# Optimization experiments

Hardware: AMD Instinct MI355X
Metric: run time of the kernel (lower is better)

The kernel has to match this reference:

```python
import jax, jax.numpy as jnp
import numpy as np

NB, M, FIN = 8, 32768, 32       # batch, mesh vertices, input features
RANK, FILT = 5, 32              # Chebyshev order, output filters
E = 262144                      # nnz of rescaled Laplacian (~8 per row)


def setup_inputs() -> dict:
    key = jax.random.key(0)
    ks = jax.random.split(key, 6)
    x = jax.random.normal(ks[0], (NB, M, FIN), dtype=jnp.float32)
    rows = jax.random.randint(ks[1], (E,), 0, M, dtype=jnp.int32)
    cols = jax.random.randint(ks[2], (E,), 0, M, dtype=jnp.int32)
    # rescaled-Laplacian values, roughly spectral-normalized
    vals = jax.random.normal(ks[3], (E,), dtype=jnp.float32) * np.float32(1.0 / np.sqrt(8.0))
    kernel = jax.random.normal(ks[4], (FIN * RANK, FILT), dtype=jnp.float32) * np.float32(0.05)
    bias = jnp.zeros((FILT,), dtype=jnp.float32)
    return {"x": x, "vals": vals, "kernel": kernel, "bias": bias, "rows": rows, "cols": cols}


def _spmm(rows, cols, vals, x0):
    # y[m, f, n] = sum_j L[m, j] * x0[j, f, n]   (COO SpMM via gather + segment_sum)
    g = vals[:, None, None] * x0[cols]           # [E, Fin, N]
    return jax.ops.segment_sum(g, rows, num_segments=x0.shape[0])


def reference(x, vals, kernel, bias, rows, cols):
    N, Mm, Fin = x.shape
    x0 = jnp.transpose(x, (1, 2, 0))             # [M, Fin, N]
    xs = [x0]
    x1 = x0
    if RANK > 1:
        x1 = _spmm(rows, cols, vals, x0)         # T_1 = L x
        xs.append(x1)
    for _ in range(2, RANK):                     # T_k = 2 L T_{k-1} - T_{k-2}
        x2 = 2.0 * _spmm(rows, cols, vals, x1) - x0
        xs.append(x2)
        x0, x1 = x1, x2
    xk = jnp.stack(xs, axis=0)                   # [K, M, Fin, N]
    xk = jnp.transpose(xk, (3, 1, 2, 0)).reshape(N * Mm, Fin * RANK)  # Fin-major, rank inner
    out = xk @ kernel + bias                     # [N*M, FILT]
    return out.reshape(N, Mm, FILT)
```

## Files before the change

### kernel.cpp

```cpp
#include <hip/hip_runtime.h>

#define M_VERT 32768
#define NBATCH 8
#define FIN 32
#define RANK 5
#define FILT 32
#define E_NNZ 262144
#define ROWLEN 256
#define EPAD (E_NNZ + 7 * M_VERT)

typedef short short8 __attribute__((ext_vector_type(8)));
typedef float f32x4 __attribute__((ext_vector_type(4)));

__device__ __forceinline__ float bfl(unsigned int u) {
    unsigned int x = u << 16; return __builtin_bit_cast(float, x);
}
__device__ __forceinline__ float bfh(unsigned int u) {
    unsigned int x = u & 0xffff0000u; return __builtin_bit_cast(float, x);
}
__device__ __forceinline__ unsigned int f2bf(float f) {
    unsigned int x = __builtin_bit_cast(unsigned int, f);
    return (x + 0x7fffu + ((x >> 16) & 1u)) >> 16;
}
__device__ __forceinline__ unsigned int pk(float a, float b) {
    return f2bf(a) | (f2bf(b) << 16);
}


__global__ void hist_kernel(const int* __restrict__ rows, int* __restrict__ cnt) {
    int e = blockIdx.x * blockDim.x + threadIdx.x;
    if (e < E_NNZ) atomicAdd(&cnt[rows[e]], 1);
}

__global__ __launch_bounds__(1024) void scan_kernel(const int* __restrict__ cnt,
                                                    int* __restrict__ rp,
                                                    int* __restrict__ fill) {
    __shared__ int sums[1024];
    int t = threadIdx.x;
    int base = t * 32;
    int local[32];
    int s = 0;
#pragma unroll
    for (int i = 0; i < 32; ++i) {
        int c = (cnt[base + i] + 7) & ~7;
        local[i] = c; s += c;
    }
    sums[t] = s;
    __syncthreads();
    for (int off = 1; off < 1024; off <<= 1) {
        int add = (t >= off) ? sums[t - off] : 0;
        __syncthreads();
        sums[t] += add;
        __syncthreads();
    }
    int pre = (t == 0) ? 0 : sums[t - 1];
#pragma unroll
    for (int i = 0; i < 32; ++i) { rp[base + i] = pre; pre += local[i]; }
    if (t == 1023) rp[M_VERT] = pre;
#pragma unroll
    for (int i = 0; i < 32; ++i) fill[base + i] = 0;
}

__global__ void scatter_kernel(const int* __restrict__ rows, const int* __restrict__ cols,
                               const float* __restrict__ vals, const int* __restrict__ rp,
                               int* __restrict__ fill, int2* __restrict__ ev) {
    int e = blockIdx.x * blockDim.x + threadIdx.x;
    if (e < E_NNZ) {
        int r = rows[e];
        int pos = rp[r] + atomicAdd(&fill[r], 1);
        int2 p; p.x = cols[e]; p.y = __builtin_bit_cast(int, vals[e]);
        ev[pos] = p;
    }
}


__global__ void pack_kernel(const float* __restrict__ x, unsigned short* __restrict__ T0) {
    int tid = blockIdx.x * blockDim.x + threadIdx.x;
    int m = tid >> 5;
    int r = tid & 31;
    int n = r >> 2;
    int q = r & 3;
    const float* src = x + ((size_t)n * M_VERT + m) * FIN + q * 8;
    float4 v0 = *(const float4*)(src);
    float4 v1 = *(const float4*)(src + 4);
    uint4 u;
    u.x = pk(v0.x, v0.y); u.y = pk(v0.z, v0.w);
    u.z = pk(v1.x, v1.y); u.w = pk(v1.z, v1.w);
    *(uint4*)(T0 + (size_t)m * ROWLEN + n * FIN + q * 8) = u;
}


__global__ void packw_kernel(const float* __restrict__ W, unsigned short* __restrict__ Wb) {
    int idx = blockIdx.x * blockDim.x + threadIdx.x;
    if (idx >= 640) return;
    int lane = idx & 63;
    int kf = idx >> 6;
    int k = kf >> 1, ft = kf & 1;
    int f = ft * 16 + (lane & 15);
    int fin0 = (lane >> 4) * 8;
    unsigned short tmp[8];
#pragma unroll
    for (int j = 0; j < 8; ++j)
        tmp[j] = (unsigned short)f2bf(W[((fin0 + j) * RANK + k) * FILT + f]);
    uint4 u;
    u.x = (unsigned int)tmp[0] | ((unsigned int)tmp[1] << 16);
    u.y = (unsigned int)tmp[2] | ((unsigned int)tmp[3] << 16);
    u.z = (unsigned int)tmp[4] | ((unsigned int)tmp[5] << 16);
    u.w = (unsigned int)tmp[6] | ((unsigned int)tmp[7] << 16);
    *(uint4*)(Wb + (size_t)idx * 8) = u;
}


__global__ __launch_bounds__(256) void spmm_kernel(const int* __restrict__ rp,
                                                   const int2* __restrict__ ev,
                                                   const unsigned short* __restrict__ Tin,
                                                   const unsigned short* __restrict__ Tsub,
                                                   unsigned short* __restrict__ Tout, int cheb) {
    int w = threadIdx.x >> 6;
    int l = threadIdx.x & 63;
    int m = blockIdx.x * 4 + w;
    int col = l * 4;
    int s = __builtin_amdgcn_readfirstlane(rp[m]);
    int e = __builtin_amdgcn_readfirstlane(rp[m + 1]);
    float a0 = 0.f, a1 = 0.f, a2 = 0.f, a3 = 0.f;
    for (int j = s; j < e; j += 8) {
        int2 ed[8];
        uint2 t[8];
#pragma unroll
        for (int i = 0; i < 8; ++i) ed[i] = ev[j + i];
#pragma unroll
        for (int i = 0; i < 8; ++i)
            t[i] = *(const uint2*)(Tin + (size_t)ed[i].x * ROWLEN + col);
#pragma unroll
        for (int i = 0; i < 8; ++i) {
            float v = __builtin_bit_cast(float, ed[i].y);
            a0 += v * bfl(t[i].x); a1 += v * bfh(t[i].x);
            a2 += v * bfl(t[i].y); a3 += v * bfh(t[i].y);
        }
    }
    if (cheb) {
        uint2 o = *(const uint2*)(Tsub + (size_t)m * ROWLEN + col);
        a0 = 2.f * a0 - bfl(o.x); a1 = 2.f * a1 - bfh(o.x);
        a2 = 2.f * a2 - bfl(o.y); a3 = 2.f * a3 - bfh(o.y);
    }
    uint2 r;
    r.x = pk(a0, a1); r.y = pk(a2, a3);
    *(uint2*)(Tout + (size_t)m * ROWLEN + col) = r;
}


__global__ __launch_bounds__(256) void gemm_kernel(const unsigned short* __restrict__ T0,
                                                   const unsigned short* __restrict__ T1,
                                                   const unsigned short* __restrict__ T2,
                                                   const unsigned short* __restrict__ T3,
                                                   const unsigned short* __restrict__ T4,
                                                   const unsigned short* __restrict__ Wb,
                                                   const float* __restrict__ bias,
                                                   float* __restrict__ out) {
    int w = threadIdx.x >> 6;
    int l = threadIdx.x & 63;
    int n  = blockIdx.x & 7;
    int mb = blockIdx.x >> 3;
    int m0 = (mb * 4 + w) * 16;
    int lrow = l & 15;
    int quad = l >> 4;

    short8 bfrag[5][2];
#pragma unroll
    for (int kf = 0; kf < 10; ++kf)
        bfrag[kf >> 1][kf & 1] = *(const short8*)(Wb + ((size_t)kf * 64 + l) * 8);

    float b0 = bias[lrow];
    float b1 = bias[16 + lrow];

    const unsigned short* Ts[5] = {T0, T1, T2, T3, T4};
    size_t abase = (size_t)(m0 + lrow) * ROWLEN + quad * 8 + n * FIN;

    f32x4 c0 = {0.f, 0.f, 0.f, 0.f};
    f32x4 c1 = {0.f, 0.f, 0.f, 0.f};
#pragma unroll
    for (int k = 0; k < 5; ++k) {
        short8 a = *(const short8*)(Ts[k] + abase);
        c0 = __builtin_amdgcn_mfma_f32_16x16x32_bf16(a, bfrag[k][0], c0, 0, 0, 0);
        c1 = __builtin_amdgcn_mfma_f32_16x16x32_bf16(a, bfrag[k][1], c1, 0, 0, 0);
    }
    float* op = out + ((size_t)n * M_VERT + m0) * FILT;
#pragma unroll
    for (int r = 0; r < 4; ++r) {
        int orow = quad * 4 + r;
        op[(size_t)orow * FILT + lrow]      = c0[r] + b0;
        op[(size_t)orow * FILT + 16 + lrow] = c1[r] + b1;
    }
}


extern "C" void kernel_launch(void* const* d_in, const int* in_sizes, int n_in,
                              void* d_out, int out_size, void* d_ws, size_t ws_size,
                              hipStream_t stream) {
    const float* x    = (const float*)d_in[0];
    const float* vals = (const float*)d_in[1];
    const float* W    = (const float*)d_in[2];
    const float* bias = (const float*)d_in[3];
    const int*   rows = (const int*)d_in[4];
    const int*   cols = (const int*)d_in[5];
    float* out = (float*)d_out;

    const size_t TSZ = (size_t)M_VERT * ROWLEN;
    unsigned short* T0 = (unsigned short*)d_ws;
    unsigned short* T1 = T0 + TSZ;
    unsigned short* T2 = T1 + TSZ;
    unsigned short* T3 = T2 + TSZ;
    unsigned short* T4 = T3 + TSZ;
    int*  rp   = (int*)(T4 + TSZ);
    int*  fill = rp + (M_VERT + 2);
    int2* ev   = (int2*)(fill + M_VERT);
    unsigned short* Wb = (unsigned short*)(ev + EPAD);

    hipMemsetAsync(fill, 0, M_VERT * sizeof(int), stream);
    hipMemsetAsync(ev, 0, (size_t)EPAD * sizeof(int2), stream);
    hist_kernel<<<E_NNZ / 256, 256, 0, stream>>>(rows, fill);
    scan_kernel<<<1, 1024, 0, stream>>>(fill, rp, fill);
    scatter_kernel<<<E_NNZ / 256, 256, 0, stream>>>(rows, cols, vals, rp, fill, ev);
    packw_kernel<<<3, 256, 0, stream>>>(W, Wb);
    pack_kernel<<<M_VERT * 32 / 256, 256, 0, stream>>>(x, T0);

    spmm_kernel<<<M_VERT / 4, 256, 0, stream>>>(rp, ev, T0, T0, T1, 0);
    spmm_kernel<<<M_VERT / 4, 256, 0, stream>>>(rp, ev, T1, T0, T2, 1);
    spmm_kernel<<<M_VERT / 4, 256, 0, stream>>>(rp, ev, T2, T1, T3, 1);
    spmm_kernel<<<M_VERT / 4, 256, 0, stream>>>(rp, ev, T3, T2, T4, 1);

    gemm_kernel<<<(M_VERT / 64) * 8, 256, 0, stream>>>(T0, T1, T2, T3, T4, Wb, bias, out);
}
```

Measured before the change: 264.4 us.

## Switch Chebyshev intermediates to batch-major slices and per-batch SpMM gathers

```diff
diff --git a/kernel.cpp b/kernel.cpp
--- a/kernel.cpp
+++ b/kernel.cpp
@@ -6,8 +6,8 @@
 #define RANK 5
 #define FILT 32
 #define E_NNZ 262144
-#define ROWLEN 256
 #define EPAD (E_NNZ + 7 * M_VERT)
+#define SLICE ((size_t)M_VERT * FIN)
 
 typedef short short8 __attribute__((ext_vector_type(8)));
 typedef float f32x4 __attribute__((ext_vector_type(4)));
@@ -75,18 +75,14 @@
 
 
 __global__ void pack_kernel(const float* __restrict__ x, unsigned short* __restrict__ T0) {
-    int tid = blockIdx.x * blockDim.x + threadIdx.x;
-    int m = tid >> 5;
-    int r = tid & 31;
-    int n = r >> 2;
-    int q = r & 3;
-    const float* src = x + ((size_t)n * M_VERT + m) * FIN + q * 8;
+    size_t tid = (size_t)blockIdx.x * blockDim.x + threadIdx.x;
+    const float* src = x + tid * 8;
     float4 v0 = *(const float4*)(src);
     float4 v1 = *(const float4*)(src + 4);
     uint4 u;
     u.x = pk(v0.x, v0.y); u.y = pk(v0.z, v0.w);
     u.z = pk(v1.x, v1.y); u.w = pk(v1.z, v1.w);
-    *(uint4*)(T0 + (size_t)m * ROWLEN + n * FIN + q * 8) = u;
+    *(uint4*)(T0 + tid * 8) = u;
 }
 
 
@@ -111,56 +107,75 @@
 }
 
 
-__global__ __launch_bounds__(256) void spmm_kernel(const int* __restrict__ rp,
-                                                   const int2* __restrict__ ev,
-                                                   const unsigned short* __restrict__ Tin,
-                                                   const unsigned short* __restrict__ Tsub,
-                                                   unsigned short* __restrict__ Tout, int cheb) {
+__global__ __launch_bounds__(256) void spmmn_kernel(const int* __restrict__ rp,
+                                                    const int2* __restrict__ ev,
+                                                    const unsigned short* __restrict__ Tin,
+                                                    const unsigned short* __restrict__ Tsub,
+                                                    unsigned short* __restrict__ Tout, int cheb) {
+    int t = threadIdx.x;
+    int g = t >> 3;
+    int p = t & 7;
+    int n  = blockIdx.x >> 10;
+    int rb = blockIdx.x & 1023;
+    int m = rb * 32 + g;
+    const unsigned short* Tn = Tin + (size_t)n * SLICE;
+    int s = rp[m], e = rp[m + 1];
+    float a0 = 0.f, a1 = 0.f, a2 = 0.f, a3 = 0.f;
+    for (int j = s; j < e; j += 8) {
+        uint4 e0 = *(const uint4*)(ev + j);
+        uint4 e1 = *(const uint4*)(ev + j + 2);
+        uint4 e2 = *(const uint4*)(ev + j + 4);
+        uint4 e3 = *(const uint4*)(ev + j + 6);
+        uint2 t0 = *(const uint2*)(Tn + (size_t)e0.x * FIN + p * 4);
+        uint2 t1 = *(const uint2*)(Tn + (size_t)e0.z * FIN + p * 4);
+        uint2 t2 = *(const uint2*)(Tn + (size_t)e1.x * FIN + p * 4);
+        uint2 t3 = *(const uint2*)(Tn + (size_t)e1.z * FIN + p * 4);
+        uint2 t4 = *(const uint2*)(Tn + (size_t)e2.x * FIN + p * 4);
+        uint2 t5 = *(const uint2*)(Tn + (size_t)e2.z * FIN + p * 4);
+        uint2 t6 = *(const uint2*)(Tn + (size_t)e3.x * FIN + p * 4);
+        uint2 t7 = *(const uint2*)(Tn + (size_t)e3.z * FIN + p * 4);
+        float v;
+        v = __builtin_bit_cast(float, e0.y);
+        a0 += v * bfl(t0.x); a1 += v * bfh(t0.x); a2 += v * bfl(t0.y); a3 += v * bfh(t0.y);
+        v = __builtin_bit_cast(float, e0.w);
+        a0 += v * bfl(t1.x); a1 += v * bfh(t1.x); a2 += v * bfl(t1.y); a3 += v * bfh(t1.y);
+        v = __builtin_bit_cast(float, e1.y);
+        a0 += v * bfl(t2.x); a1 += v * bfh(t2.x); a2 += v * bfl(t2.y); a3 += v * bfh(t2.y);
+        v = __builtin_bit_cast(float, e1.w);
+        a0 += v * bfl(t3.x); a1 += v * bfh(t3.x); a2 += v * bfl(t3.y); a3 += v * bfh(t3.y);
+        v = __builtin_bit_cast(float, e2.y);
+        a0 += v * bfl(t4.x); a1 += v * bfh(t4.x); a2 += v * bfl(t4.y); a3 += v * bfh(t4.y);
+        v = __builtin_bit_cast(float, e2.w);
+        a0 += v * bfl(t5.x); a1 += v * bfh(t5.x); a2 += v * bfl(t5.y); a3 += v * bfh(t5.y);
+        v = __builtin_bit_cast(float, e3.y);
+        a0 += v * bfl(t6.x); a1 += v * bfh(t6.x); a2 += v * bfl(t6.y); a3 += v * bfh(t6.y);
+        v = __builtin_bit_cast(float, e3.w);
+        a0 += v * bfl(t7.x); a1 += v * bfh(t7.x); a2 += v * bfl(t7.y); a3 += v * bfh(t7.y);
+    }
+    size_t off = (size_t)n * SLICE + (size_t)m * FIN + p * 4;
+    if (cheb) {
+        uint2 o = *(const uint2*)(Tsub + off);
+        a0 = 2.f * a0 - bfl(o.x); a1 = 2.f * a1 - bfh(o.x);
+        a2 = 2.f * a2 - bfl(o.y); a3 = 2.f * a3 - bfh(o.y);
+    }
+    uint2 r;
+    r.x = pk(a0, a1); r.y = pk(a2, a3);
+    *(uint2*)(Tout + off) = r;
+}
+
+
+__global__ __launch_bounds__(256, 4) void gemm_kernel(const unsigned short* __restrict__ T0,
+                                                      const unsigned short* __restrict__ T1,
+                                                      const unsigned short* __restrict__ T2,
+                                                      const unsigned short* __restrict__ T3,
+                                                      const unsigned short* __restrict__ T4,
+                                                      const unsigned short* __restrict__ Wb,
+                                                      const float* __restrict__ bias,
+                                                      float* __restrict__ out) {
     int w = threadIdx.x >> 6;
     int l = threadIdx.x & 63;
-    int m = blockIdx.x * 4 + w;
-    int col = l * 4;
-    int s = __builtin_amdgcn_readfirstlane(rp[m]);
-    int e = __builtin_amdgcn_readfirstlane(rp[m + 1]);
-    float a0 = 0.f, a1 = 0.f, a2 = 0.f, a3 = 0.f;
-    for (int j = s; j < e; j += 8) {
-        int2 ed[8];
-        uint2 t[8];
-#pragma unroll
-        for (int i = 0; i < 8; ++i) ed[i] = ev[j + i];
-#pragma unroll
-        for (int i = 0; i < 8; ++i)
-            t[i] = *(const uint2*)(Tin + (size_t)ed[i].x * ROWLEN + col);
-#pragma unroll
-        for (int i = 0; i < 8; ++i) {
-            float v = __builtin_bit_cast(float, ed[i].y);
-            a0 += v * bfl(t[i].x); a1 += v * bfh(t[i].x);
-            a2 += v * bfl(t[i].y); a3 += v * bfh(t[i].y);
-        }
-    }
-    if (cheb) {
-        uint2 o = *(const uint2*)(Tsub + (size_t)m * ROWLEN + col);
-        a0 = 2.f * a0 - bfl(o.x); a1 = 2.f * a1 - bfh(o.x);
-        a2 = 2.f * a2 - bfl(o.y); a3 = 2.f * a3 - bfh(o.y);
-    }
-    uint2 r;
-    r.x = pk(a0, a1); r.y = pk(a2, a3);
-    *(uint2*)(Tout + (size_t)m * ROWLEN + col) = r;
-}
-
-
-__global__ __launch_bounds__(256) void gemm_kernel(const unsigned short* __restrict__ T0,
-                                                   const unsigned short* __restrict__ T1,
-                                                   const unsigned short* __restrict__ T2,
-                                                   const unsigned short* __restrict__ T3,
-                                                   const unsigned short* __restrict__ T4,
-                                                   const unsigned short* __restrict__ Wb,
-                                                   const float* __restrict__ bias,
-                                                   float* __restrict__ out) {
-    int w = threadIdx.x >> 6;
-    int l = threadIdx.x & 63;
-    int n  = blockIdx.x & 7;
-    int mb = blockIdx.x >> 3;
+    int g  = blockIdx.x & 1;
+    int mb = blockIdx.x >> 1;
     int m0 = (mb * 4 + w) * 16;
     int lrow = l & 15;
     int quad = l >> 4;
@@ -174,22 +189,39 @@
     float b1 = bias[16 + lrow];
 
     const unsigned short* Ts[5] = {T0, T1, T2, T3, T4};
-    size_t abase = (size_t)(m0 + lrow) * ROWLEN + quad * 8 + n * FIN;
-
-    f32x4 c0 = {0.f, 0.f, 0.f, 0.f};
-    f32x4 c1 = {0.f, 0.f, 0.f, 0.f};
+    size_t rowoff = (size_t)(m0 + lrow) * FIN + quad * 8;
+
+    f32x4 c0[4], c1[4];
+#pragma unroll
+    for (int nn = 0; nn < 4; ++nn) { c0[nn] = (f32x4){0.f,0.f,0.f,0.f}; c1[nn] = (f32x4){0.f,0.f,0.f,0.f}; }
+
 #pragma unroll
     for (int k = 0; k < 5; ++k) {
-        short8 a = *(const short8*)(Ts[k] + abase);
-        c0 = __builtin_amdgcn_mfma_f32_16x16x32_bf16(a, bfrag[k][0], c0, 0, 0, 0);
-        c1 = __builtin_amdgcn_mfma_f32_16x16x32_bf16(a, bfrag[k][1], c1, 0, 0, 0);
-    }
-    float* op = out + ((size_t)n * M_VERT + m0) * FILT;
-#pragma unroll
-    for (int r = 0; r < 4; ++r) {
-        int orow = quad * 4 + r;
-        op[(size_t)orow * FILT + lrow]      = c0[r] + b0;
-        op[(size_t)orow * FILT + 16 + lrow] = c1[r] + b1;
+        const unsigned short* p = Ts[k] + rowoff + (size_t)g * 4 * SLICE;
+        short8 a0 = *(const short8*)(p);
+        short8 a1 = *(const short8*)(p + SLICE);
+        short8 a2 = *(const short8*)(p + 2 * SLICE);
+        short8 a3 = *(const short8*)(p + 3 * SLICE);
+        c0[0] = __builtin_amdgcn_mfma_f32_16x16x32_bf16(a0, bfrag[k][0], c0[0], 0, 0, 0);
+        c1[0] = __builtin_amdgcn_mfma_f32_16x16x32_bf16(a0, bfrag[k][1], c1[0], 0, 0, 0);
+        c0[1] = __builtin_amdgcn_mfma_f32_16x16x32_bf16(a1, bfrag[k][0], c0[1], 0, 0, 0);
+        c1[1] = __builtin_amdgcn_mfma_f32_16x16x32_bf16(a1, bfrag[k][1], c1[1], 0, 0, 0);
+        c0[2] = __builtin_amdgcn_mfma_f32_16x16x32_bf16(a2, bfrag[k][0], c0[2], 0, 0, 0);
+        c1[2] = __builtin_amdgcn_mfma_f32_16x16x32_bf16(a2, bfrag[k][1], c1[2], 0, 0, 0);
+        c0[3] = __builtin_amdgcn_mfma_f32_16x16x32_bf16(a3, bfrag[k][0], c0[3], 0, 0, 0);
+        c1[3] = __builtin_amdgcn_mfma_f32_16x16x32_bf16(a3, bfrag[k][1], c1[3], 0, 0, 0);
+    }
+
+#pragma unroll
+    for (int nn = 0; nn < 4; ++nn) {
+        int n = g * 4 + nn;
+        float* op = out + ((size_t)n * M_VERT + m0) * FILT;
+#pragma unroll
+        for (int r = 0; r < 4; ++r) {
+            int orow = quad * 4 + r;
+            op[(size_t)orow * FILT + lrow]      = c0[nn][r] + b0;
+            op[(size_t)orow * FILT + 16 + lrow] = c1[nn][r] + b1;
+        }
     }
 }
 
@@ -205,7 +237,7 @@
     const int*   cols = (const int*)d_in[5];
     float* out = (float*)d_out;
 
-    const size_t TSZ = (size_t)M_VERT * ROWLEN;
+    const size_t TSZ = (size_t)NBATCH * SLICE;
     unsigned short* T0 = (unsigned short*)d_ws;
     unsigned short* T1 = T0 + TSZ;
     unsigned short* T2 = T1 + TSZ;
@@ -213,7 +245,7 @@
     unsigned short* T4 = T3 + TSZ;
     int*  rp   = (int*)(T4 + TSZ);
     int*  fill = rp + (M_VERT + 2);
-    int2* ev   = (int2*)(fill + M_VERT);
+    int2* ev   = (int2*)(((uintptr_t)(fill + M_VERT) + 15) & ~(uintptr_t)15);
     unsigned short* Wb = (unsigned short*)(ev + EPAD);
 
     hipMemsetAsync(fill, 0, M_VERT * sizeof(int), stream);
@@ -222,12 +254,12 @@
     scan_kernel<<<1, 1024, 0, stream>>>(fill, rp, fill);
     scatter_kernel<<<E_NNZ / 256, 256, 0, stream>>>(rows, cols, vals, rp, fill, ev);
     packw_kernel<<<3, 256, 0, stream>>>(W, Wb);
-    pack_kernel<<<M_VERT * 32 / 256, 256, 0, stream>>>(x, T0);
-
-    spmm_kernel<<<M_VERT / 4, 256, 0, stream>>>(rp, ev, T0, T0, T1, 0);
-    spmm_kernel<<<M_VERT / 4, 256, 0, stream>>>(rp, ev, T1, T0, T2, 1);
-    spmm_kernel<<<M_VERT / 4, 256, 0, stream>>>(rp, ev, T2, T1, T3, 1);
-    spmm_kernel<<<M_VERT / 4, 256, 0, stream>>>(rp, ev, T3, T2, T4, 1);
-
-    gemm_kernel<<<(M_VERT / 64) * 8, 256, 0, stream>>>(T0, T1, T2, T3, T4, Wb, bias, out);
-}
+    pack_kernel<<<(NBATCH * M_VERT * FIN / 8) / 256, 256, 0, stream>>>(x, T0);
+
+    spmmn_kernel<<<NBATCH * 1024, 256, 0, stream>>>(rp, ev, T0, T0, T1, 0);
+    spmmn_kernel<<<NBATCH * 1024, 256, 0, stream>>>(rp, ev, T1, T0, T2, 1);
+    spmmn_kernel<<<NBATCH * 1024, 256, 0, stream>>>(rp, ev, T2, T1, T3, 1);
+    spmmn_kernel<<<NBATCH * 1024, 256, 0, stream>>>(rp, ev, T3, T2, T4, 1);
+
+    gemm_kernel<<<(M_VERT / 64) * 2, 256, 0, stream>>>(T0, T1, T2, T3, T4, Wb, bias, out);
+}
```

Measured after the change: 273.1 us. 3.3% more time.
